# Kernel optimization log

Measured on AMD Instinct MI355X. Metric: run time of the kernel, lower is better.

## Reference

```python
import jax, jax.numpy as jnp
import numpy as np
from jax import lax

N = 8192
D = 64

def setup_inputs() -> dict:
    key = jax.random.key(0)
    k1, k2 = jax.random.split(key)
    nodevec1 = jax.random.normal(k1, (N, D), dtype=jnp.float32)
    nodevec2 = jax.random.normal(k2, (D, N), dtype=jnp.float32)
    return {"nodevec1": nodevec1, "nodevec2": nodevec2, "topk": 32}

def reference(nodevec1, nodevec2, topk):
    # [N, N] low-rank adjacency
    adp = jnp.maximum(nodevec1 @ nodevec2, 0.0)
    n = adp.shape[1]
    if topk < n:
        # per-row top-k, scatter values into zeros (matches torch.topk + scatter_)
        vals, idx = lax.top_k(adp, topk)  # [N, k]
        rows = jnp.arange(adp.shape[0])[:, None]  # [N, 1]
        adp = jnp.zeros_like(adp).at[rows, idx].set(vals)
    # softmax over full row, zeros included (exp(0)=1 terms), same as F.softmax
    return jax.nn.softmax(adp, axis=1)
```

## Files before the change

kernel.cpp:

```cpp
#include <hip/hip_runtime.h>

#define NN 8192
#define DD 64
#define ROWS 16
#define NWAVE 16
#define K2NT 1024
#define TPW 32
#define CAP 320
#define NBINS 160
#define INVBINW 4.0f
#define SHIFT 48.0f
#define ZSCALE 4503599627370496.0f
#define SELCAP 64
#define K3NT 256
#define K3ROWS 4

typedef _Float16 half8 __attribute__((ext_vector_type(8)));
typedef float    f32x4 __attribute__((ext_vector_type(4)));

__device__ __forceinline__ unsigned h16bits(_Float16 h) {
    union { _Float16 h; unsigned short u; } cv; cv.h = h; return (unsigned)cv.u;
}
__device__ __forceinline__ float h16val(unsigned u) {
    union { unsigned short u; _Float16 h; } cv; cv.u = (unsigned short)u; return (float)cv.h;
}

__global__ __launch_bounds__(256) void prep_bt(
    const float* __restrict__ in, _Float16* __restrict__ bt2)
{
    __shared__ float t[64][65];
    const int c0 = blockIdx.x * 64;
    for (int i = threadIdx.x; i < 4096; i += 256) {
        const int r = i >> 6, c = i & 63;
        t[c][r] = in[(size_t)r * NN + c0 + c];
    }
    __syncthreads();
    for (int i = threadIdx.x; i < 4096; i += 256) {
        const int c = i >> 6, r = i & 63;
        const int col = c0 + c;
        const int dst = ((col >> 4) * 2 + (r >> 5)) * 512
                      + (((r >> 3) & 3) * 16 + (col & 15)) * 8 + (r & 7);
        bt2[dst] = (_Float16)t[c][r];
    }
}

__global__ __launch_bounds__(K2NT) void sag_sel(
    const float* __restrict__ nv1, const _Float16* __restrict__ bt2,
    const int* __restrict__ topkp,
    float* __restrict__ rowb0, int* __restrict__ rowcnt,
    unsigned long long* __restrict__ sellist)
{
    __shared__ unsigned int       cand[ROWS][CAP];
    __shared__ unsigned int       hist[ROWS][NBINS];
    __shared__ unsigned long long sel[ROWS][SELCAP];
    __shared__ unsigned long long zfx[ROWS];
    __shared__ int   ccnt[ROWS];
    __shared__ int   ecnt[ROWS];
    __shared__ int   bsel_i[ROWS];
    __shared__ float iZ_f[ROWS];
    __shared__ float norm2[16];

    const int tid = threadIdx.x, wv = tid >> 6, ln = tid & 63;
    const int g = ln >> 4, cl = ln & 15;
    const int row0 = blockIdx.x * ROWS;
    const int K = topkp[0];

    for (int i = tid; i < ROWS * NBINS; i += K2NT) (&hist[0][0])[i] = 0u;
    if (tid < ROWS) { ccnt[tid] = 0; ecnt[tid] = 0; zfx[tid] = 0ull; }

    half8 af[2];
    float s2 = 0.f;
    {
        const float* pa = nv1 + (size_t)(row0 + cl) * DD + g * 8;
        #pragma unroll
        for (int ks = 0; ks < 2; ++ks)
            #pragma unroll
            for (int j = 0; j < 8; ++j) {
                const float x = pa[ks * 32 + j];
                af[ks][j] = (_Float16)x;
                s2 += x * x;
            }
    }
    s2 += __shfl_xor(s2, 16);
    s2 += __shfl_xor(s2, 32);
    if (wv == 0 && ln < 16) norm2[ln] = s2;
    __syncthreads();

    float pref4[4];
    #pragma unroll
    for (int i = 0; i < 4; ++i) pref4[i] = 2.0f * sqrtf(norm2[g * 4 + i]);

    const _Float16* pb = bt2 + (size_t)(wv * TPW) * 1024 + ln * 8;
    const int wbase = wv * 512;

    #pragma unroll 4
    for (int t = 0; t < TPW; ++t) {
        const half8 b0 = *reinterpret_cast<const half8*>(pb + t * 1024);
        const half8 b1 = *reinterpret_cast<const half8*>(pb + t * 1024 + 512);
        f32x4 acc = {0.f, 0.f, 0.f, 0.f};
        acc = __builtin_amdgcn_mfma_f32_16x16x32_f16(af[0], b0, acc, 0, 0, 0);
        acc = __builtin_amdgcn_mfma_f32_16x16x32_f16(af[1], b1, acc, 0, 0, 0);
        #pragma unroll
        for (int i = 0; i < 4; ++i) {
            const float v = fmaxf(acc[i], 0.f);
            if (v > pref4[i]) {
                const int r = g * 4 + i;
                const unsigned key = (h16bits((_Float16)v) << 13)
                                   | (unsigned)(wbase + t * 16 + cl);
                const int idx = atomicAdd(&ccnt[r], 1);
                if (idx < CAP) cand[r][idx] = key;
            }
        }
    }
    __syncthreads();

    {
        const int n = min(ccnt[wv], CAP);
        for (int idx = ln; idx < n; idx += 64) {
            const float vb = h16val(cand[wv][idx] >> 13);
            int bi = (int)(vb * INVBINW);
            bi = bi < NBINS - 1 ? bi : NBINS - 1;
            atomicAdd(&hist[wv][bi], 1u);
        }
    }
    __syncthreads();

    if (tid < ROWS) {
        int cum = 0, bsel = 0;
        for (int b = NBINS - 1; b >= 0; --b) {
            cum += (int)hist[tid][b];
            if (cum >= K) { bsel = b; break; }
        }
        bsel_i[tid] = bsel;
    }
    __syncthreads();

    {
        const int n  = min(ccnt[wv], CAP);
        const int bs = bsel_i[wv];
        for (int idx = ln; idx < n; idx += 64) {
            const unsigned key = cand[wv][idx];
            const float vb = h16val(key >> 13);
            int bi = (int)(vb * INVBINW);
            bi = bi < NBINS - 1 ? bi : NBINS - 1;
            if (bi >= bs) {
                const float e = __expf(vb - SHIFT);
                atomicAdd(&zfx[wv], (unsigned long long)(e * ZSCALE));
                const int slot = atomicAdd(&ecnt[wv], 1);
                if (slot < SELCAP)
                    sel[wv][slot] = ((unsigned long long)__float_as_uint(e) << 32)
                                  | (key & 0x1FFFu);
            }
        }
    }
    __syncthreads();

    if (tid < ROWS) {
        const int cnt = min(ecnt[tid], SELCAP);
        const float e0 = __expf(-SHIFT);
        const float Z  = ldexpf((float)zfx[tid], -52) + (float)(NN - cnt) * e0;
        const float iZ = 1.0f / Z;
        iZ_f[tid] = iZ;
        rowb0[row0 + tid] = e0 * iZ;
        rowcnt[row0 + tid] = cnt;
    }
    __syncthreads();

    {
        const int r = tid >> 6, s = tid & 63;
        if (s < min(ecnt[r], SELCAP)) {
            const unsigned long long w = sel[r][s];
            const float ov = __uint_as_float((unsigned)(w >> 32)) * iZ_f[r];
            sellist[(size_t)(row0 + r) * SELCAP + s] =
                ((unsigned long long)__float_as_uint(ov) << 32) | (unsigned)(w & 0x1FFFu);
        }
    }
}

__global__ __launch_bounds__(K3NT) void sag_fill(
    const float* __restrict__ rowb0, const int* __restrict__ rowcnt,
    const unsigned long long* __restrict__ sellist, float* __restrict__ out)
{
    const int r0 = blockIdx.x * K3ROWS;
    const int tid = threadIdx.x;
    #pragma unroll
    for (int r = 0; r < K3ROWS; ++r) {
        const float b0 = rowb0[r0 + r];
        const f32x4 bv = {b0, b0, b0, b0};
        f32x4* po = reinterpret_cast<f32x4*>(out + (size_t)(r0 + r) * NN);
        #pragma unroll
        for (int q = 0; q < NN / 4 / K3NT; ++q) po[q * K3NT + tid] = bv;
    }
    __syncthreads();
    const int r = tid >> 6, s = tid & 63;
    if (s < rowcnt[r0 + r]) {
        const unsigned long long w = sellist[(size_t)(r0 + r) * SELCAP + s];
        out[(size_t)(r0 + r) * NN + (unsigned)(w & 0x1FFFu)] =
            __uint_as_float((unsigned)(w >> 32));
    }
}

extern "C" void kernel_launch(void* const* d_in, const int* in_sizes, int n_in,
                              void* d_out, int out_size, void* d_ws, size_t ws_size,
                              hipStream_t stream) {
    const float* nv1   = (const float*)d_in[0];
    const float* nv2   = (const float*)d_in[1];
    const int*   topkp = (const int*)d_in[2];
    float*       out   = (float*)d_out;

    char* ws = (char*)d_ws;
    _Float16*           bt2     = (_Float16*)ws;
    float*              rowb0   = (float*)(ws + (1 << 20));
    int*                rowcnt  = (int*)(ws + (1 << 20) + (32 << 10));
    unsigned long long* sellist = (unsigned long long*)(ws + (1 << 20) + (64 << 10));

    hipLaunchKernelGGL(prep_bt, dim3(NN / 64),        dim3(256),  0, stream, nv2, bt2);
    hipLaunchKernelGGL(sag_sel, dim3(NN / ROWS),      dim3(K2NT), 0, stream,
                       nv1, bt2, topkp, rowb0, rowcnt, sellist);
    hipLaunchKernelGGL(sag_fill, dim3(NN / K3ROWS),   dim3(K3NT), 0, stream,
                       rowb0, rowcnt, sellist, out);
}
```

Before: 94.85 us.

## Fuse fill kernel into selection kernel and parallelize histogram threshold scan

The separate fill kernel is folded into the selection kernel, so each block writes its 16 output rows directly: a background fill followed by a scatter of the top-k softmax values. This drops one launch and the round trip of per-row base values and selected lists through global memory. The serial per-row histogram scan is also replaced by a wave-level prefix sum with ballot to find the threshold bin. The cost is a fused kernel that must hold its heavy shared-memory footprint while doing the large output write, which may reduce overlap of compute and stores across blocks.

```diff
diff --git a/kernel.cpp b/kernel.cpp
--- a/kernel.cpp
+++ b/kernel.cpp
@@ -12,8 +12,6 @@
 #define SHIFT 48.0f
 #define ZSCALE 4503599627370496.0f
 #define SELCAP 64
-#define K3NT 256
-#define K3ROWS 4
 
 typedef _Float16 half8 __attribute__((ext_vector_type(8)));
 typedef float    f32x4 __attribute__((ext_vector_type(4)));
@@ -44,11 +42,9 @@
     }
 }
 
-__global__ __launch_bounds__(K2NT) void sag_sel(
+__global__ __launch_bounds__(K2NT) void sag_fused(
     const float* __restrict__ nv1, const _Float16* __restrict__ bt2,
-    const int* __restrict__ topkp,
-    float* __restrict__ rowb0, int* __restrict__ rowcnt,
-    unsigned long long* __restrict__ sellist)
+    const int* __restrict__ topkp, float* __restrict__ out)
 {
     __shared__ unsigned int       cand[ROWS][CAP];
     __shared__ unsigned int       hist[ROWS][NBINS];
@@ -58,6 +54,7 @@
     __shared__ int   ecnt[ROWS];
     __shared__ int   bsel_i[ROWS];
     __shared__ float iZ_f[ROWS];
+    __shared__ float b0_f[ROWS];
     __shared__ float norm2[16];
 
     const int tid = threadIdx.x, wv = tid >> 6, ln = tid & 63;
@@ -125,13 +122,30 @@
     }
     __syncthreads();
 
-    if (tid < ROWS) {
-        int cum = 0, bsel = 0;
-        for (int b = NBINS - 1; b >= 0; --b) {
-            cum += (int)hist[tid][b];
-            if (cum >= K) { bsel = b; break; }
-        }
-        bsel_i[tid] = bsel;
+    {
+        const int r = wv;
+        unsigned s0 = hist[r][159 - ln];
+        unsigned s1 = hist[r][95 - ln];
+        unsigned s2b = (ln < 32) ? hist[r][31 - ln] : 0u;
+        #pragma unroll
+        for (int d = 1; d < 64; d <<= 1) {
+            const unsigned t0 = __shfl_up(s0, d);
+            const unsigned t1 = __shfl_up(s1, d);
+            const unsigned t2 = __shfl_up(s2b, d);
+            if (ln >= d) { s0 += t0; s1 += t1; s2b += t2; }
+        }
+        const unsigned tot0 = __shfl(s0, 63);
+        const unsigned tot1 = __shfl(s1, 63);
+        s1 += tot0;
+        s2b += tot0 + tot1;
+        const unsigned long long m0 = __ballot(s0 >= (unsigned)K);
+        const unsigned long long m1 = __ballot(s1 >= (unsigned)K);
+        const unsigned long long m2 = __ballot(s2b >= (unsigned)K);
+        int bsel = 0;
+        if (m0)      bsel = 159 - (__ffsll(m0) - 1);
+        else if (m1) bsel = 95  - (__ffsll(m1) - 1);
+        else if (m2) bsel = 31  - (__ffsll(m2) - 1);
+        if (ln == 0) bsel_i[r] = bsel;
     }
     __syncthreads();
 
@@ -161,42 +175,28 @@
         const float Z  = ldexpf((float)zfx[tid], -52) + (float)(NN - cnt) * e0;
         const float iZ = 1.0f / Z;
         iZ_f[tid] = iZ;
-        rowb0[row0 + tid] = e0 * iZ;
-        rowcnt[row0 + tid] = cnt;
+        b0_f[tid] = e0 * iZ;
+        ecnt[tid] = cnt;
+    }
+    __syncthreads();
+
+    #pragma unroll
+    for (int r = 0; r < ROWS; ++r) {
+        const float b0 = b0_f[r];
+        const f32x4 bv = {b0, b0, b0, b0};
+        f32x4* po = reinterpret_cast<f32x4*>(out + (size_t)(row0 + r) * NN);
+        po[tid]        = bv;
+        po[tid + K2NT] = bv;
     }
     __syncthreads();
 
     {
         const int r = tid >> 6, s = tid & 63;
-        if (s < min(ecnt[r], SELCAP)) {
+        if (s < ecnt[r]) {
             const unsigned long long w = sel[r][s];
             const float ov = __uint_as_float((unsigned)(w >> 32)) * iZ_f[r];
-            sellist[(size_t)(row0 + r) * SELCAP + s] =
-                ((unsigned long long)__float_as_uint(ov) << 32) | (unsigned)(w & 0x1FFFu);
-        }
-    }
-}
-
-__global__ __launch_bounds__(K3NT) void sag_fill(
-    const float* __restrict__ rowb0, const int* __restrict__ rowcnt,
-    const unsigned long long* __restrict__ sellist, float* __restrict__ out)
-{
-    const int r0 = blockIdx.x * K3ROWS;
-    const int tid = threadIdx.x;
-    #pragma unroll
-    for (int r = 0; r < K3ROWS; ++r) {
-        const float b0 = rowb0[r0 + r];
-        const f32x4 bv = {b0, b0, b0, b0};
-        f32x4* po = reinterpret_cast<f32x4*>(out + (size_t)(r0 + r) * NN);
-        #pragma unroll
-        for (int q = 0; q < NN / 4 / K3NT; ++q) po[q * K3NT + tid] = bv;
-    }
-    __syncthreads();
-    const int r = tid >> 6, s = tid & 63;
-    if (s < rowcnt[r0 + r]) {
-        const unsigned long long w = sellist[(size_t)(r0 + r) * SELCAP + s];
-        out[(size_t)(r0 + r) * NN + (unsigned)(w & 0x1FFFu)] =
-            __uint_as_float((unsigned)(w >> 32));
+            out[(size_t)(row0 + r) * NN + (unsigned)(w & 0x1FFFu)] = ov;
+        }
     }
 }
 
@@ -207,16 +207,9 @@
     const float* nv2   = (const float*)d_in[1];
     const int*   topkp = (const int*)d_in[2];
     float*       out   = (float*)d_out;
-
-    char* ws = (char*)d_ws;
-    _Float16*           bt2     = (_Float16*)ws;
-    float*              rowb0   = (float*)(ws + (1 << 20));
-    int*                rowcnt  = (int*)(ws + (1 << 20) + (32 << 10));
-    unsigned long long* sellist = (unsigned long long*)(ws + (1 << 20) + (64 << 10));
-
-    hipLaunchKernelGGL(prep_bt, dim3(NN / 64),        dim3(256),  0, stream, nv2, bt2);
-    hipLaunchKernelGGL(sag_sel, dim3(NN / ROWS),      dim3(K2NT), 0, stream,
-                       nv1, bt2, topkp, rowb0, rowcnt, sellist);
-    hipLaunchKernelGGL(sag_fill, dim3(NN / K3ROWS),   dim3(K3NT), 0, stream,
-                       rowb0, rowcnt, sellist, out);
-}
+    _Float16*    bt2   = (_Float16*)d_ws;
+
+    hipLaunchKernelGGL(prep_bt,   dim3(NN / 64),   dim3(256),  0, stream, nv2, bt2);
+    hipLaunchKernelGGL(sag_fused, dim3(NN / ROWS), dim3(K2NT), 0, stream,
+                       nv1, bt2, topkp, out);
+}
```

After: 90.12 us. 1.05x faster.
